# Kernel optimization log

Hardware: AMD Instinct MI355X
Metric: run time of the kernel (lower is better)

## Reference

```python
import jax, jax.numpy as jnp
import numpy as np

NEG = -1e9


def setup_inputs() -> dict:
    key = jax.random.key(0)
    kq, kk, kv, ke = jax.random.split(key, 4)
    B, H, S, D = 4, 16, 2048, 64
    q = jax.random.normal(kq, (B, H, S, D), dtype=jnp.float32)
    k = jax.random.normal(kk, (B, H, S, D), dtype=jnp.float32)
    v = jax.random.normal(kv, (B, H, S, D), dtype=jnp.float32)
    event_length = jax.random.randint(ke, (B,), 0, S, dtype=jnp.int32)
    return {"q": q, "k": k, "v": v, "event_length": event_length}


def reference(q, k, v, event_length):
    B, H, S, D = q.shape
    scale = jnp.sqrt(jnp.asarray(D, dtype=jnp.float32))
    # [b,h,s,q] scores
    scores = jnp.einsum('bhsd,bhqd->bhsq', q, k) / scale
    idx = jnp.arange(S)
    el = event_length[:, None]  # [B,1]
    valid = idx[None, :] < el   # [B,S]
    # mask[b,s,q] = valid[b,s] & valid[b,q]; broadcast over heads
    mask = (valid[:, None, :, None] & valid[:, None, None, :])  # [B,1,S,S]
    scores = jnp.where(mask, scores, NEG)
    attn = jax.nn.softmax(scores, axis=-1)
    # dropout p=0.0 (eval): identity
    out = jnp.einsum('bhsq,bhqd->bhsd', attn, v)
    return out
```

## Files before the change

### kernel.cpp

```cpp
#include <hip/hip_runtime.h>
#include <hip/hip_bf16.h>


#define SQ 2048
#define DH 64
#define NBH 64
#define TK 64
#define NTILE 32
#define TILE_B 8192
#define LDE 72
#define LVP 68

typedef __attribute__((ext_vector_type(4))) float f32x4;
typedef __attribute__((ext_vector_type(8))) short bf16x8;
typedef __attribute__((ext_vector_type(4))) unsigned int u32x4;
typedef __attribute__((ext_vector_type(2))) unsigned int u32x2;

__device__ __forceinline__ unsigned int pk2(float lo, float hi) {
    __hip_bfloat162 h = __float22bfloat162_rn(float2{lo, hi});
    union { __hip_bfloat162 h; unsigned int u; } c; c.h = h;
    return c.u;
}

__device__ __forceinline__ float bfu16_to_f(unsigned short s) {
    union { unsigned int u; float f; } c; c.u = ((unsigned int)s) << 16;
    return c.f;
}

__device__ __forceinline__ void async_cp16(const void* g, void* l) {
    __builtin_amdgcn_global_load_lds(
        (const __attribute__((address_space(1))) unsigned int*)g,
        (__attribute__((address_space(3))) unsigned int*)l, 16, 0, 0);
}


__global__ __launch_bounds__(256)
void convkv(const float* __restrict__ K, const float* __restrict__ V,
            const int* __restrict__ EL, float* __restrict__ MV,
            char* __restrict__ Kbt, char* __restrict__ Vbt) {
    const int bh = blockIdx.x >> 5;
    const int kt = blockIdx.x & 31;
    const int k0 = kt * TK;
    const int el = EL[bh >> 4];
    const int t = threadIdx.x;
    const int r  = t >> 2;
    const int dc = t & 3;

    __shared__ short LV[64][LVP];

    {
        const float* vp = V + ((size_t)bh * SQ + k0 + r) * DH + dc * 16;
        f32x4 a = *(const f32x4*)vp;
        f32x4 b = *(const f32x4*)(vp + 4);
        f32x4 c2 = *(const f32x4*)(vp + 8);
        f32x4 d2 = *(const f32x4*)(vp + 12);
        u32x4 w0, w1;
        w0[0] = pk2(a[0], a[1]);  w0[1] = pk2(a[2], a[3]);
        w0[2] = pk2(b[0], b[1]);  w0[3] = pk2(b[2], b[3]);
        w1[0] = pk2(c2[0], c2[1]); w1[1] = pk2(c2[2], c2[3]);
        w1[2] = pk2(d2[0], d2[1]); w1[3] = pk2(d2[2], d2[3]);
        *(u32x4*)&LV[r][dc * 16]     = w0;
        *(u32x4*)&LV[r][dc * 16 + 8] = w1;
    }

    if (k0 < el) {
        const float* kp = K + ((size_t)bh * SQ + k0 + r) * DH + dc * 16;
        f32x4 a = *(const f32x4*)kp;
        f32x4 b = *(const f32x4*)(kp + 4);
        f32x4 c2 = *(const f32x4*)(kp + 8);
        f32x4 d2 = *(const f32x4*)(kp + 12);
        u32x4 w0, w1;
        w0[0] = pk2(a[0], a[1]);  w0[1] = pk2(a[2], a[3]);
        w0[2] = pk2(b[0], b[1]);  w0[3] = pk2(b[2], b[3]);
        w1[0] = pk2(c2[0], c2[1]); w1[1] = pk2(c2[2], c2[3]);
        w1[2] = pk2(d2[0], d2[1]); w1[3] = pk2(d2[2], d2[3]);
        char* kb = Kbt + (size_t)(bh * NTILE + kt) * TILE_B + r * 128;
        *(u32x4*)(kb + (((dc * 2)     ^ (r & 7)) << 4)) = w0;
        *(u32x4*)(kb + (((dc * 2 + 1) ^ (r & 7)) << 4)) = w1;
    }

    __syncthreads();

    const int dd  = t >> 2;
    const int seg = t & 3;
    float msum = 0.f;
    unsigned int wv[8];
    #pragma unroll
    for (int i = 0; i < 8; ++i) {
        const int pos = seg * 16 + 2 * i;
        const int key = (pos & ~31) | ((pos & 4) << 2) | ((pos & 24) >> 1) | (pos & 3);
        const unsigned short s0 = (unsigned short)LV[key][dd];
        const unsigned short s1 = (unsigned short)LV[key + 1][dd];
        msum += bfu16_to_f(s0) + bfu16_to_f(s1);
        wv[i] = (unsigned int)s0 | ((unsigned int)s1 << 16);
    }
    msum += __shfl_xor(msum, 1);
    msum += __shfl_xor(msum, 2);
    if (seg == 0) atomicAdd(&MV[bh * DH + dd], msum * (1.0f / (float)SQ));

    if (k0 < el) {
        char* vb = Vbt + (size_t)(bh * NTILE + kt) * TILE_B + dd * 128;
        u32x4 o0 = {wv[0], wv[1], wv[2], wv[3]};
        u32x4 o1 = {wv[4], wv[5], wv[6], wv[7]};
        *(u32x4*)(vb + (((seg * 2)     ^ (dd & 7)) << 4)) = o0;
        *(u32x4*)(vb + (((seg * 2 + 1) ^ (dd & 7)) << 4)) = o1;
    }
}

__global__ __launch_bounds__(512, 4)
void flash6(const float* __restrict__ Q, const int* __restrict__ EL,
            const float* __restrict__ MV, float* __restrict__ O,
            const char* __restrict__ Kbt, const char* __restrict__ Vbt,
            int* __restrict__ ticket) {
    const int t = threadIdx.x;

    {
        const int bh0 = blockIdx.x & (NBH - 1);
        const int qb0 = (blockIdx.x >> 6) * 128;
        const int elb = EL[bh0 >> 4];
        if (qb0 >= elb) {
            float* Op = O + (size_t)bh0 * SQ * DH;
            const int c16 = t & 15, r0 = t >> 4;
            f32x4 mv = *(const f32x4*)(MV + bh0 * DH + c16 * 4);
            #pragma unroll
            for (int i = 0; i < 4; ++i)
                *(f32x4*)(Op + (size_t)(qb0 + r0 + i * 32) * DH + c16 * 4) = mv;
        }
    }

    const int el0 = EL[0], el1 = EL[1], el2 = EL[2], el3 = EL[3];
    const int v0 = (el0 + 127) >> 7, v1 = (el1 + 127) >> 7;
    const int v2 = (el2 + 127) >> 7, v3 = (el3 + 127) >> 7;
    const int n0 = 16 * v0, n1 = n0 + 16 * v1, n2 = n1 + 16 * v2;
    const int nvalid = n2 + 16 * v3;

    __shared__ short KT[2][TK * DH];
    __shared__ short VT[2][TK * DH];
    __shared__ int item_s;

    const int wq = t >> 6, lane = t & 63, qd = lane >> 4, c = lane & 15;
    const int cs = c & 7;

    for (;;) {
        if (t == 0) item_s = atomicAdd(ticket, 1);
        __syncthreads();
        const int it = item_s;
        if (it >= nvalid) break;

        int b, u, vb, el;
        if      (it < n0) { b = 0; u = it;      vb = v0; el = el0; }
        else if (it < n1) { b = 1; u = it - n0; vb = v1; el = el1; }
        else if (it < n2) { b = 2; u = it - n1; vb = v2; el = el2; }
        else              { b = 3; u = it - n2; vb = v3; el = el3; }
        const int head  = u / vb;
        const int qt    = u - head * vb;
        const int bh    = b * 16 + head;
        const int qbase = qt * 128;

        const float* Qp = Q + (size_t)bh * SQ * DH;
        float*       Op = O + (size_t)bh * SQ * DH;
        const char*  Kt = Kbt + (size_t)bh * NTILE * TILE_B;
        const char*  Vt = Vbt + (size_t)bh * NTILE * TILE_B;

        const float sc = 0.125f * 1.44269504f;
        const int qrow = qbase + wq * 16 + c;
        bf16x8 qf[2];
        #pragma unroll
        for (int kc = 0; kc < 2; ++kc) {
            const float* p = Qp + (size_t)qrow * DH + kc * 32 + qd * 8;
            f32x4 a  = *(const f32x4*)p;
            f32x4 bq = *(const f32x4*)(p + 4);
            u32x4 f;
            f[0] = pk2(a[0] * sc, a[1] * sc);
            f[1] = pk2(a[2] * sc, a[3] * sc);
            f[2] = pk2(bq[0] * sc, bq[1] * sc);
            f[3] = pk2(bq[2] * sc, bq[3] * sc);
            qf[kc] = *(bf16x8*)&f;
        }

        float l_ = 0.f;
        f32x4 oacc[4];
        #pragma unroll
        for (int dt = 0; dt < 4; ++dt) oacc[dt] = (f32x4){0.f, 0.f, 0.f, 0.f};

        const int nkt = (el + TK - 1) >> 6;

        {
            async_cp16(Kt + (size_t)t * 16, (char*)&KT[0][0] + wq * 1024);
            async_cp16(Vt + (size_t)t * 16, (char*)&VT[0][0] + wq * 1024);
        }
        asm volatile("s_waitcnt vmcnt(0)" ::: "memory");
        __syncthreads();

        int buf = 0;
        for (int kt = 0; kt < nkt; ++kt) {
            if (kt + 1 < nkt) {
                const char* gK = Kt + (size_t)(kt + 1) * TILE_B + t * 16;
                const char* gV = Vt + (size_t)(kt + 1) * TILE_B + t * 16;
                async_cp16(gK, (char*)&KT[buf ^ 1][0] + wq * 1024);
                async_cp16(gV, (char*)&VT[buf ^ 1][0] + wq * 1024);
            }
            const int k0 = kt * TK;

            const char* Kb = (const char*)&KT[buf][0];
            f32x4 st[4];
            #pragma unroll
            for (int mt = 0; mt < 4; ++mt) {
                const char* rp = Kb + (mt * 16 + c) * 128;
                bf16x8 a0 = *(const bf16x8*)(rp + (((qd)     ^ cs) << 4));
                bf16x8 a1 = *(const bf16x8*)(rp + (((qd + 4) ^ cs) << 4));
                f32x4 acc = (f32x4){0.f, 0.f, 0.f, 0.f};
                acc = __builtin_amdgcn_mfma_f32_16x16x32_bf16(a0, qf[0], acc, 0, 0, 0);
                acc = __builtin_amdgcn_mfma_f32_16x16x32_bf16(a1, qf[1], acc, 0, 0, 0);
                st[mt] = acc;
            }

            if (k0 + TK > el) {
                #pragma unroll
                for (int mt = 0; mt < 4; ++mt)
                    #pragma unroll
                    for (int r = 0; r < 4; ++r)
                        if (k0 + mt * 16 + qd * 4 + r >= el) st[mt][r] = -1e30f;
            }

            u32x4 pw[2];
            #pragma unroll
            for (int mt = 0; mt < 4; ++mt) {
                const float p0 = exp2f(st[mt][0]);
                const float p1 = exp2f(st[mt][1]);
                const float p2 = exp2f(st[mt][2]);
                const float p3 = exp2f(st[mt][3]);
                l_ += (p0 + p1) + (p2 + p3);
                pw[mt >> 1][(mt & 1) * 2]     = pk2(p0, p1);
                pw[mt >> 1][(mt & 1) * 2 + 1] = pk2(p2, p3);
            }

            const char* Vb = (const char*)&VT[buf][0];
            #pragma unroll
            for (int kc = 0; kc < 2; ++kc) {
                bf16x8 pb = *(bf16x8*)&pw[kc];
                #pragma unroll
                for (int dt = 0; dt < 4; ++dt) {
                    const char* vp = Vb + (dt * 16 + c) * 128 + (((kc * 4 + qd) ^ cs) << 4);
                    bf16x8 vf = *(const bf16x8*)vp;
                    oacc[dt] = __builtin_amdgcn_mfma_f32_16x16x32_bf16(vf, pb, oacc[dt], 0, 0, 0);
                }
            }

            asm volatile("s_waitcnt vmcnt(0)" ::: "memory");
            __syncthreads();
            buf ^= 1;
        }

        l_ += __shfl_xor(l_, 16);
        l_ += __shfl_xor(l_, 32);

        if (qrow < el) {
            const float inv = 1.0f / l_;
            #pragma unroll
            for (int dt = 0; dt < 4; ++dt) {
                f32x4 o = oacc[dt];
                o[0] *= inv; o[1] *= inv; o[2] *= inv; o[3] *= inv;
                *(f32x4*)(Op + (size_t)qrow * DH + dt * 16 + qd * 4) = o;
            }
        } else {
            #pragma unroll
            for (int dt = 0; dt < 4; ++dt)
                *(f32x4*)(Op + (size_t)qrow * DH + dt * 16 + qd * 4) =
                    *(const f32x4*)(MV + bh * DH + dt * 16 + qd * 4);
        }
    }
}


__global__ __launch_bounds__(256)
void meanv_k(const float* __restrict__ V, float* __restrict__ MV) {
    const int bh  = blockIdx.x >> 4;
    const int seg = blockIdx.x & 15;
    const float* vp = V + ((size_t)bh * SQ + (size_t)seg * 128) * DH;
    const int c = threadIdx.x & 15;
    const int r = threadIdx.x >> 4;
    const float* p = vp + (size_t)r * DH + c * 4;
    f32x4 s0 = *(const f32x4*)(p);
    f32x4 s1 = *(const f32x4*)(p + 16 * DH);
    f32x4 s2 = *(const f32x4*)(p + 32 * DH);
    f32x4 s3 = *(const f32x4*)(p + 48 * DH);
    s0 += *(const f32x4*)(p + 64 * DH);
    s1 += *(const f32x4*)(p + 80 * DH);
    s2 += *(const f32x4*)(p + 96 * DH);
    s3 += *(const f32x4*)(p + 112 * DH);
    f32x4 s = (s0 + s1) + (s2 + s3);
    __shared__ f32x4 red[16][16];
    red[r][c] = s;
    __syncthreads();
    if (threadIdx.x < 16) {
        f32x4 a = red[0][threadIdx.x];
        #pragma unroll
        for (int j = 1; j < 16; ++j) a += red[j][threadIdx.x];
        const float inv = 1.0f / (float)SQ;
        atomicAdd(&MV[bh * DH + threadIdx.x * 4 + 0], a[0] * inv);
        atomicAdd(&MV[bh * DH + threadIdx.x * 4 + 1], a[1] * inv);
        atomicAdd(&MV[bh * DH + threadIdx.x * 4 + 2], a[2] * inv);
        atomicAdd(&MV[bh * DH + threadIdx.x * 4 + 3], a[3] * inv);
    }
}

__global__ __launch_bounds__(256, 3)
void flash5(const float* __restrict__ Q, const float* __restrict__ K,
            const float* __restrict__ V, const int* __restrict__ EL,
            const float* __restrict__ MV, float* __restrict__ O,
            int* __restrict__ ticket) {
    const int t = threadIdx.x;
    {
        const int bh0    = blockIdx.x & (NBH - 1);
        const int qbase0 = (blockIdx.x >> 6) * 128;
        const int elb    = EL[bh0 >> 4];
        if (qbase0 >= elb) {
            float* Op = O + (size_t)bh0 * SQ * DH;
            const int c16 = t & 15, r0 = t >> 4;
            f32x4 mv = *(const f32x4*)(MV + bh0 * DH + c16 * 4);
            #pragma unroll
            for (int i = 0; i < 8; ++i)
                *(f32x4*)(Op + (size_t)(qbase0 + r0 + i * 16) * DH + c16 * 4) = mv;
        }
    }

    const int el0 = EL[0], el1 = EL[1], el2 = EL[2], el3 = EL[3];
    const int v0 = (el0 + 127) >> 7, v1 = (el1 + 127) >> 7;
    const int v2 = (el2 + 127) >> 7, v3 = (el3 + 127) >> 7;
    const int n0 = 16 * v0, n1 = n0 + 16 * v1, n2 = n1 + 16 * v2;
    const int nvalid = n2 + 16 * v3;

    __shared__ short Kb[TK][LDE];
    __shared__ short Vt[DH][LDE];
    __shared__ short Pl[4][32][LDE];
    __shared__ int item_s;

    const int wq = t >> 6, lane = t & 63, qd = lane >> 4, c = lane & 15;
    const int ksrow = t >> 2;
    const int ksdc  = t & 3;
    const int vpair = t & 31;
    const int vdg   = t >> 5;

    for (;;) {
        if (t == 0) item_s = atomicAdd(ticket, 1);
        __syncthreads();
        const int it = item_s;
        if (it >= nvalid) break;

        int b, u, vb, el;
        if      (it < n0) { b = 0; u = it;      vb = v0; el = el0; }
        else if (it < n1) { b = 1; u = it - n0; vb = v1; el = el1; }
        else if (it < n2) { b = 2; u = it - n1; vb = v2; el = el2; }
        else              { b = 3; u = it - n2; vb = v3; el = el3; }
        const int head  = u / vb;
        const int qt    = u - head * vb;
        const int bh    = b * 16 + head;
        const int qbase = qt * 128;

        const size_t base = (size_t)bh * SQ * DH;
        const float* Qp = Q + base;
        const float* Kp = K + base;
        const float* Vp = V + base;
        float* Op = O + base;

        const float sc = 0.125f * 1.44269504f;
        bf16x8 qf[2][2];
        #pragma unroll
        for (int nt = 0; nt < 2; ++nt) {
            const int row = qbase + wq * 32 + nt * 16 + c;
            #pragma unroll
            for (int kc = 0; kc < 2; ++kc) {
                const float* p = Qp + (size_t)row * DH + kc * 32 + qd * 8;
                f32x4 a  = *(const f32x4*)p;
                f32x4 bb = *(const f32x4*)(p + 4);
                u32x4 f;
                f[0] = pk2(a[0] * sc, a[1] * sc);
                f[1] = pk2(a[2] * sc, a[3] * sc);
                f[2] = pk2(bb[0] * sc, bb[1] * sc);
                f[3] = pk2(bb[2] * sc, bb[3] * sc);
                qf[nt][kc] = *(bf16x8*)&f;
            }
        }

        float l_[2] = {0.f, 0.f};
        f32x4 oacc[4][2];
        #pragma unroll
        for (int dt = 0; dt < 4; ++dt)
            #pragma unroll
            for (int nt = 0; nt < 2; ++nt)
                oacc[dt][nt] = (f32x4){0.f, 0.f, 0.f, 0.f};

        const int nkt = (el + TK - 1) / TK;

        f32x4 kg0, kg1, kg2, kg3, vg0, vg1, vg2, vg3;
        {
            const float* kp = Kp + (size_t)ksrow * DH + ksdc * 16;
            kg0 = *(const f32x4*)kp;
            kg1 = *(const f32x4*)(kp + 4);
            kg2 = *(const f32x4*)(kp + 8);
            kg3 = *(const f32x4*)(kp + 12);
            const float* vp0 = Vp + (size_t)(2 * vpair) * DH + vdg * 8;
            vg0 = *(const f32x4*)vp0;
            vg1 = *(const f32x4*)(vp0 + 4);
            vg2 = *(const f32x4*)(vp0 + DH);
            vg3 = *(const f32x4*)(vp0 + DH + 4);
        }

        for (int kt = 0; kt < nkt; ++kt) {
            const int k0 = kt * TK;

            __syncthreads();
            {
                u32x4 w0, w1;
                w0[0] = pk2(kg0[0], kg0[1]); w0[1] = pk2(kg0[2], kg0[3]);
                w0[2] = pk2(kg1[0], kg1[1]); w0[3] = pk2(kg1[2], kg1[3]);
                w1[0] = pk2(kg2[0], kg2[1]); w1[1] = pk2(kg2[2], kg2[3]);
                w1[2] = pk2(kg3[0], kg3[1]); w1[3] = pk2(kg3[2], kg3[3]);
                *(u32x4*)&Kb[ksrow][ksdc * 16]     = w0;
                *(u32x4*)&Kb[ksrow][ksdc * 16 + 8] = w1;
            }
            {
                #pragma unroll
                for (int i = 0; i < 4; ++i) {
                    *(unsigned int*)&Vt[vdg * 8 + i][2 * vpair]     = pk2(vg0[i], vg2[i]);
                    *(unsigned int*)&Vt[vdg * 8 + 4 + i][2 * vpair] = pk2(vg1[i], vg3[i]);
                }
            }
            __syncthreads();

            if (kt + 1 < nkt) {
                const int kn = k0 + TK;
                const float* kp = Kp + (size_t)(kn + ksrow) * DH + ksdc * 16;
                kg0 = *(const f32x4*)kp;
                kg1 = *(const f32x4*)(kp + 4);
                kg2 = *(const f32x4*)(kp + 8);
                kg3 = *(const f32x4*)(kp + 12);
                const float* vp0 = Vp + (size_t)(kn + 2 * vpair) * DH + vdg * 8;
                vg0 = *(const f32x4*)vp0;
                vg1 = *(const f32x4*)(vp0 + 4);
                vg2 = *(const f32x4*)(vp0 + DH);
                vg3 = *(const f32x4*)(vp0 + DH + 4);
            }

            f32x4 st[4][2];
            #pragma unroll
            for (int mt = 0; mt < 4; ++mt) {
                bf16x8 a0 = *(const bf16x8*)&Kb[mt * 16 + c][qd * 8];
                bf16x8 a1 = *(const bf16x8*)&Kb[mt * 16 + c][32 + qd * 8];
                #pragma unroll
                for (int nt = 0; nt < 2; ++nt) {
                    f32x4 acc = (f32x4){0.f, 0.f, 0.f, 0.f};
                    acc = __builtin_amdgcn_mfma_f32_16x16x32_bf16(a0, qf[nt][0], acc, 0, 0, 0);
                    acc = __builtin_amdgcn_mfma_f32_16x16x32_bf16(a1, qf[nt][1], acc, 0, 0, 0);
                    st[mt][nt] = acc;
                }
            }

            if (k0 + TK > el) {
                #pragma unroll
                for (int mt = 0; mt < 4; ++mt)
                    #pragma unroll
                    for (int r = 0; r < 4; ++r)
                        if (k0 + mt * 16 + qd * 4 + r >= el) {
                            st[mt][0][r] = -1e30f;
                            st[mt][1][r] = -1e30f;
                        }
            }

            #pragma unroll
            for (int nt = 0; nt < 2; ++nt) {
                #pragma unroll
                for (int mt = 0; mt < 4; ++mt) {
                    const float p0 = exp2f(st[mt][nt][0]);
                    const float p1 = exp2f(st[mt][nt][1]);
                    const float p2 = exp2f(st[mt][nt][2]);
                    const float p3 = exp2f(st[mt][nt][3]);
                    l_[nt] += (p0 + p1) + (p2 + p3);
                    u32x2 pw;
                    pw[0] = pk2(p0, p1);
                    pw[1] = pk2(p2, p3);
                    *(u32x2*)&Pl[wq][nt * 16 + c][mt * 16 + qd * 4] = pw;
                }
            }

            #pragma unroll
            for (int kc = 0; kc < 2; ++kc) {
                bf16x8 pb0 = *(const bf16x8*)&Pl[wq][c][kc * 32 + qd * 8];
                bf16x8 pb1 = *(const bf16x8*)&Pl[wq][16 + c][kc * 32 + qd * 8];
                #pragma unroll
                for (int dt = 0; dt < 4; ++dt) {
                    bf16x8 vf = *(const bf16x8*)&Vt[dt * 16 + c][kc * 32 + qd * 8];
                    oacc[dt][0] = __builtin_amdgcn_mfma_f32_16x16x32_bf16(vf, pb0, oacc[dt][0], 0, 0, 0);
                    oacc[dt][1] = __builtin_amdgcn_mfma_f32_16x16x32_bf16(vf, pb1, oacc[dt][1], 0, 0, 0);
                }
            }
        }

        #pragma unroll
        for (int nt = 0; nt < 2; ++nt) {
            l_[nt] += __shfl_xor(l_[nt], 16);
            l_[nt] += __shfl_xor(l_[nt], 32);
        }

        #pragma unroll
        for (int nt = 0; nt < 2; ++nt) {
            const int row = qbase + wq * 32 + nt * 16 + c;
            if (row < el) {
                const float inv = 1.0f / l_[nt];
                #pragma unroll
                for (int dt = 0; dt < 4; ++dt) {
                    f32x4 o = oacc[dt][nt];
                    o[0] *= inv; o[1] *= inv; o[2] *= inv; o[3] *= inv;
                    *(f32x4*)(Op + (size_t)row * DH + dt * 16 + qd * 4) = o;
                }
            } else {
                #pragma unroll
                for (int dt = 0; dt < 4; ++dt) {
                    f32x4 mv = *(const f32x4*)(MV + bh * DH + dt * 16 + qd * 4);
                    *(f32x4*)(Op + (size_t)row * DH + dt * 16 + qd * 4) = mv;
                }
            }
        }
    }
}


extern "C" void kernel_launch(void* const* d_in, const int* in_sizes, int n_in,
                              void* d_out, int out_size, void* d_ws, size_t ws_size,
                              hipStream_t stream) {
    const float* q  = (const float*)d_in[0];
    const float* k  = (const float*)d_in[1];
    const float* v  = (const float*)d_in[2];
    const int*   el = (const int*)d_in[3];
    float* out = (float*)d_out;

    const size_t kbt_bytes = (size_t)NBH * NTILE * TILE_B;
    const size_t needed    = 65536 + 2 * kbt_bytes;

    if (ws_size >= needed) {
        float* mv  = (float*)d_ws;
        int*   tk  = (int*)((char*)d_ws + 16384);
        char*  kbt = (char*)d_ws + 65536;
        char*  vbt = kbt + kbt_bytes;

        hipMemsetAsync(d_ws, 0, 65536, stream);
        convkv<<<dim3(NBH * NTILE), dim3(256), 0, stream>>>(k, v, el, mv, kbt, vbt);
        flash6<<<dim3(NBH * (SQ / 128)), dim3(512), 0, stream>>>(q, el, mv, out, kbt, vbt, tk);
    } else {
        float* mv = (float*)d_ws;
        int*   tk = (int*)((char*)d_ws + NBH * DH * sizeof(float));

        hipMemsetAsync(d_ws, 0, NBH * DH * sizeof(float) + 64, stream);
        meanv_k<<<dim3(NBH * 16), dim3(256), 0, stream>>>(v, mv);
        flash5<<<dim3(NBH * (SQ / 128)), dim3(256), 0, stream>>>(q, k, v, el, mv, out, tk);
    }
}
```

Measured before the change: 194.2 us.

## Process two query sub-tiles per wave with 256-thread blocks to reuse K/V fragments

Each wave now handles 32 query rows (two 16-row sub-tiles) instead of 16, and the block shrinks from 512 to 256 threads. Every K and V fragment read from LDS feeds two MFMAs, halving LDS reads per unit of compute, and each thread issues two async copies per tile to keep the 64-key K/V tile fully loaded. The softmax exp also switches to the raw hardware exp2 builtin. Costs are higher register pressure (twice the accumulators, scores and Q fragments) and fewer waves per block to hide latency.

```diff
diff --git a/kernel.cpp b/kernel.cpp
--- a/kernel.cpp
+++ b/kernel.cpp
@@ -107,8 +107,8 @@
     }
 }
 
-__global__ __launch_bounds__(512, 4)
-void flash6(const float* __restrict__ Q, const int* __restrict__ EL,
+__global__ __launch_bounds__(256, 4)
+void flash7(const float* __restrict__ Q, const int* __restrict__ EL,
             const float* __restrict__ MV, float* __restrict__ O,
             const char* __restrict__ Kbt, const char* __restrict__ Vbt,
             int* __restrict__ ticket) {
@@ -123,8 +123,8 @@
             const int c16 = t & 15, r0 = t >> 4;
             f32x4 mv = *(const f32x4*)(MV + bh0 * DH + c16 * 4);
             #pragma unroll
-            for (int i = 0; i < 4; ++i)
-                *(f32x4*)(Op + (size_t)(qb0 + r0 + i * 32) * DH + c16 * 4) = mv;
+            for (int i = 0; i < 8; ++i)
+                *(f32x4*)(Op + (size_t)(qb0 + r0 + i * 16) * DH + c16 * 4) = mv;
         }
     }
 
@@ -163,31 +163,39 @@
         const char*  Vt = Vbt + (size_t)bh * NTILE * TILE_B;
 
         const float sc = 0.125f * 1.44269504f;
-        const int qrow = qbase + wq * 16 + c;
-        bf16x8 qf[2];
-        #pragma unroll
-        for (int kc = 0; kc < 2; ++kc) {
-            const float* p = Qp + (size_t)qrow * DH + kc * 32 + qd * 8;
-            f32x4 a  = *(const f32x4*)p;
-            f32x4 bq = *(const f32x4*)(p + 4);
-            u32x4 f;
-            f[0] = pk2(a[0] * sc, a[1] * sc);
-            f[1] = pk2(a[2] * sc, a[3] * sc);
-            f[2] = pk2(bq[0] * sc, bq[1] * sc);
-            f[3] = pk2(bq[2] * sc, bq[3] * sc);
-            qf[kc] = *(bf16x8*)&f;
-        }
-
-        float l_ = 0.f;
-        f32x4 oacc[4];
-        #pragma unroll
-        for (int dt = 0; dt < 4; ++dt) oacc[dt] = (f32x4){0.f, 0.f, 0.f, 0.f};
+        bf16x8 qf[2][2];
+        #pragma unroll
+        for (int nt = 0; nt < 2; ++nt) {
+            const int row = qbase + wq * 32 + nt * 16 + c;
+            #pragma unroll
+            for (int kc = 0; kc < 2; ++kc) {
+                const float* p = Qp + (size_t)row * DH + kc * 32 + qd * 8;
+                f32x4 a  = *(const f32x4*)p;
+                f32x4 bq = *(const f32x4*)(p + 4);
+                u32x4 f;
+                f[0] = pk2(a[0] * sc, a[1] * sc);
+                f[1] = pk2(a[2] * sc, a[3] * sc);
+                f[2] = pk2(bq[0] * sc, bq[1] * sc);
+                f[3] = pk2(bq[2] * sc, bq[3] * sc);
+                qf[nt][kc] = *(bf16x8*)&f;
+            }
+        }
+
+        float l_[2] = {0.f, 0.f};
+        f32x4 oacc[4][2];
+        #pragma unroll
+        for (int dt = 0; dt < 4; ++dt) {
+            oacc[dt][0] = (f32x4){0.f, 0.f, 0.f, 0.f};
+            oacc[dt][1] = (f32x4){0.f, 0.f, 0.f, 0.f};
+        }
 
         const int nkt = (el + TK - 1) >> 6;
 
         {
-            async_cp16(Kt + (size_t)t * 16, (char*)&KT[0][0] + wq * 1024);
-            async_cp16(Vt + (size_t)t * 16, (char*)&VT[0][0] + wq * 1024);
+            async_cp16(Kt + (size_t)t * 16,        (char*)&KT[0][0] + wq * 1024);
+            async_cp16(Kt + 4096 + (size_t)t * 16, (char*)&KT[0][0] + 4096 + wq * 1024);
+            async_cp16(Vt + (size_t)t * 16,        (char*)&VT[0][0] + wq * 1024);
+            async_cp16(Vt + 4096 + (size_t)t * 16, (char*)&VT[0][0] + 4096 + wq * 1024);
         }
         asm volatile("s_waitcnt vmcnt(0)" ::: "memory");
         __syncthreads();
@@ -197,22 +205,29 @@
             if (kt + 1 < nkt) {
                 const char* gK = Kt + (size_t)(kt + 1) * TILE_B + t * 16;
                 const char* gV = Vt + (size_t)(kt + 1) * TILE_B + t * 16;
-                async_cp16(gK, (char*)&KT[buf ^ 1][0] + wq * 1024);
-                async_cp16(gV, (char*)&VT[buf ^ 1][0] + wq * 1024);
+                char* lK = (char*)&KT[buf ^ 1][0] + wq * 1024;
+                char* lV = (char*)&VT[buf ^ 1][0] + wq * 1024;
+                async_cp16(gK,        lK);
+                async_cp16(gK + 4096, lK + 4096);
+                async_cp16(gV,        lV);
+                async_cp16(gV + 4096, lV + 4096);
             }
             const int k0 = kt * TK;
 
             const char* Kb = (const char*)&KT[buf][0];
-            f32x4 st[4];
+            f32x4 st[4][2];
             #pragma unroll
             for (int mt = 0; mt < 4; ++mt) {
                 const char* rp = Kb + (mt * 16 + c) * 128;
                 bf16x8 a0 = *(const bf16x8*)(rp + (((qd)     ^ cs) << 4));
                 bf16x8 a1 = *(const bf16x8*)(rp + (((qd + 4) ^ cs) << 4));
-                f32x4 acc = (f32x4){0.f, 0.f, 0.f, 0.f};
-                acc = __builtin_amdgcn_mfma_f32_16x16x32_bf16(a0, qf[0], acc, 0, 0, 0);
-                acc = __builtin_amdgcn_mfma_f32_16x16x32_bf16(a1, qf[1], acc, 0, 0, 0);
-                st[mt] = acc;
+                #pragma unroll
+                for (int nt = 0; nt < 2; ++nt) {
+                    f32x4 acc = (f32x4){0.f, 0.f, 0.f, 0.f};
+                    acc = __builtin_amdgcn_mfma_f32_16x16x32_bf16(a0, qf[nt][0], acc, 0, 0, 0);
+                    acc = __builtin_amdgcn_mfma_f32_16x16x32_bf16(a1, qf[nt][1], acc, 0, 0, 0);
+                    st[mt][nt] = acc;
+                }
             }
 
             if (k0 + TK > el) {
@@ -220,30 +235,38 @@
                 for (int mt = 0; mt < 4; ++mt)
                     #pragma unroll
                     for (int r = 0; r < 4; ++r)
-                        if (k0 + mt * 16 + qd * 4 + r >= el) st[mt][r] = -1e30f;
-            }
-
-            u32x4 pw[2];
-            #pragma unroll
-            for (int mt = 0; mt < 4; ++mt) {
-                const float p0 = exp2f(st[mt][0]);
-                const float p1 = exp2f(st[mt][1]);
-                const float p2 = exp2f(st[mt][2]);
-                const float p3 = exp2f(st[mt][3]);
-                l_ += (p0 + p1) + (p2 + p3);
-                pw[mt >> 1][(mt & 1) * 2]     = pk2(p0, p1);
-                pw[mt >> 1][(mt & 1) * 2 + 1] = pk2(p2, p3);
+                        if (k0 + mt * 16 + qd * 4 + r >= el) {
+                            st[mt][0][r] = -1e30f;
+                            st[mt][1][r] = -1e30f;
+                        }
+            }
+
+            u32x4 pw[2][2];
+            #pragma unroll
+            for (int nt = 0; nt < 2; ++nt) {
+                #pragma unroll
+                for (int mt = 0; mt < 4; ++mt) {
+                    const float p0 = __builtin_amdgcn_exp2f(st[mt][nt][0]);
+                    const float p1 = __builtin_amdgcn_exp2f(st[mt][nt][1]);
+                    const float p2 = __builtin_amdgcn_exp2f(st[mt][nt][2]);
+                    const float p3 = __builtin_amdgcn_exp2f(st[mt][nt][3]);
+                    l_[nt] += (p0 + p1) + (p2 + p3);
+                    pw[nt][mt >> 1][(mt & 1) * 2]     = pk2(p0, p1);
+                    pw[nt][mt >> 1][(mt & 1) * 2 + 1] = pk2(p2, p3);
+                }
             }
 
             const char* Vb = (const char*)&VT[buf][0];
             #pragma unroll
             for (int kc = 0; kc < 2; ++kc) {
-                bf16x8 pb = *(bf16x8*)&pw[kc];
+                bf16x8 pb0 = *(bf16x8*)&pw[0][kc];
+                bf16x8 pb1 = *(bf16x8*)&pw[1][kc];
                 #pragma unroll
                 for (int dt = 0; dt < 4; ++dt) {
                     const char* vp = Vb + (dt * 16 + c) * 128 + (((kc * 4 + qd) ^ cs) << 4);
                     bf16x8 vf = *(const bf16x8*)vp;
-                    oacc[dt] = __builtin_amdgcn_mfma_f32_16x16x32_bf16(vf, pb, oacc[dt], 0, 0, 0);
+                    oacc[dt][0] = __builtin_amdgcn_mfma_f32_16x16x32_bf16(vf, pb0, oacc[dt][0], 0, 0, 0);
+                    oacc[dt][1] = __builtin_amdgcn_mfma_f32_16x16x32_bf16(vf, pb1, oacc[dt][1], 0, 0, 0);
                 }
             }
 
@@ -252,22 +275,29 @@
             buf ^= 1;
         }
 
-        l_ += __shfl_xor(l_, 16);
-        l_ += __shfl_xor(l_, 32);
-
-        if (qrow < el) {
-            const float inv = 1.0f / l_;
-            #pragma unroll
-            for (int dt = 0; dt < 4; ++dt) {
-                f32x4 o = oacc[dt];
-                o[0] *= inv; o[1] *= inv; o[2] *= inv; o[3] *= inv;
-                *(f32x4*)(Op + (size_t)qrow * DH + dt * 16 + qd * 4) = o;
-            }
-        } else {
-            #pragma unroll
-            for (int dt = 0; dt < 4; ++dt)
-                *(f32x4*)(Op + (size_t)qrow * DH + dt * 16 + qd * 4) =
-                    *(const f32x4*)(MV + bh * DH + dt * 16 + qd * 4);
+        #pragma unroll
+        for (int nt = 0; nt < 2; ++nt) {
+            l_[nt] += __shfl_xor(l_[nt], 16);
+            l_[nt] += __shfl_xor(l_[nt], 32);
+        }
+
+        #pragma unroll
+        for (int nt = 0; nt < 2; ++nt) {
+            const int qrow = qbase + wq * 32 + nt * 16 + c;
+            if (qrow < el) {
+                const float inv = 1.0f / l_[nt];
+                #pragma unroll
+                for (int dt = 0; dt < 4; ++dt) {
+                    f32x4 o = oacc[dt][nt];
+                    o[0] *= inv; o[1] *= inv; o[2] *= inv; o[3] *= inv;
+                    *(f32x4*)(Op + (size_t)qrow * DH + dt * 16 + qd * 4) = o;
+                }
+            } else {
+                #pragma unroll
+                for (int dt = 0; dt < 4; ++dt)
+                    *(f32x4*)(Op + (size_t)qrow * DH + dt * 16 + qd * 4) =
+                        *(const f32x4*)(MV + bh * DH + dt * 16 + qd * 4);
+            }
         }
     }
 }
@@ -546,7 +576,7 @@
 
         hipMemsetAsync(d_ws, 0, 65536, stream);
         convkv<<<dim3(NBH * NTILE), dim3(256), 0, stream>>>(k, v, el, mv, kbt, vbt);
-        flash6<<<dim3(NBH * (SQ / 128)), dim3(512), 0, stream>>>(q, el, mv, out, kbt, vbt, tk);
+        flash7<<<dim3(NBH * (SQ / 128)), dim3(256), 0, stream>>>(q, el, mv, out, kbt, vbt, tk);
     } else {
         float* mv = (float*)d_ws;
         int*   tk = (int*)((char*)d_ws + NBH * DH * sizeof(float));
```

After: 197.2 us. About the same (+1.6%).

## Triple-buffer K/V tiles with fragment-ordered layout and prefetch depth two

Applied to the files above, without the earlier changes.

The K/V conversion kernel now writes tiles in MFMA fragment order, so each lane reads its operands with contiguous 16-byte loads at fixed offsets and no XOR swizzle. The flash kernel moves from double to triple-buffered LDS with two tiles in flight and partial vmcnt waits. It also issues the first loads before the Q fragment setup, raises the occupancy hint, uses the raw exp2 builtin and brackets the MFMA blocks with setprio. The aim is to hide global-to-LDS latency and cut LDS address math, at the cost of 48KB of LDS per block, which may limit occupancy, and an extra barrier per iteration.

```diff
diff --git a/kernel.cpp b/kernel.cpp
--- a/kernel.cpp
+++ b/kernel.cpp
@@ -15,6 +15,8 @@
 typedef __attribute__((ext_vector_type(8))) short bf16x8;
 typedef __attribute__((ext_vector_type(4))) unsigned int u32x4;
 typedef __attribute__((ext_vector_type(2))) unsigned int u32x2;
+
+#define VMCNT(n) asm volatile("s_waitcnt vmcnt(" #n ")" ::: "memory")
 
 __device__ __forceinline__ unsigned int pk2(float lo, float hi) {
     __hip_bfloat162 h = __float22bfloat162_rn(float2{lo, hi});
@@ -74,9 +76,12 @@
         w0[2] = pk2(b[0], b[1]);  w0[3] = pk2(b[2], b[3]);
         w1[0] = pk2(c2[0], c2[1]); w1[1] = pk2(c2[2], c2[3]);
         w1[2] = pk2(d2[0], d2[1]); w1[3] = pk2(d2[2], d2[3]);
-        char* kb = Kbt + (size_t)(bh * NTILE + kt) * TILE_B + r * 128;
-        *(u32x4*)(kb + (((dc * 2)     ^ (r & 7)) << 4)) = w0;
-        *(u32x4*)(kb + (((dc * 2 + 1) ^ (r & 7)) << 4)) = w1;
+        char* kb = Kbt + (size_t)(bh * NTILE + kt) * TILE_B;
+        const int fi  = (r >> 4) * 2 + (dc >> 1);
+        const int qd0 = (dc & 1) * 2;
+        char* d0 = kb + fi * 1024 + qd0 * 256 + (r & 15) * 16;
+        *(u32x4*)d0         = w0;
+        *(u32x4*)(d0 + 256) = w1;
     }
 
     __syncthreads();
@@ -99,16 +104,19 @@
     if (seg == 0) atomicAdd(&MV[bh * DH + dd], msum * (1.0f / (float)SQ));
 
     if (k0 < el) {
-        char* vb = Vbt + (size_t)(bh * NTILE + kt) * TILE_B + dd * 128;
+        char* vbb = Vbt + (size_t)(bh * NTILE + kt) * TILE_B;
+        const int fi  = (seg >> 1) * 4 + (dd >> 4);
+        const int qd0 = (seg & 1) * 2;
+        char* d0 = vbb + fi * 1024 + qd0 * 256 + (dd & 15) * 16;
         u32x4 o0 = {wv[0], wv[1], wv[2], wv[3]};
         u32x4 o1 = {wv[4], wv[5], wv[6], wv[7]};
-        *(u32x4*)(vb + (((seg * 2)     ^ (dd & 7)) << 4)) = o0;
-        *(u32x4*)(vb + (((seg * 2 + 1) ^ (dd & 7)) << 4)) = o1;
-    }
-}
-
-__global__ __launch_bounds__(512, 4)
-void flash6(const float* __restrict__ Q, const int* __restrict__ EL,
+        *(u32x4*)d0         = o0;
+        *(u32x4*)(d0 + 256) = o1;
+    }
+}
+
+__global__ __launch_bounds__(512, 6)
+void flash9(const float* __restrict__ Q, const int* __restrict__ EL,
             const float* __restrict__ MV, float* __restrict__ O,
             const char* __restrict__ Kbt, const char* __restrict__ Vbt,
             int* __restrict__ ticket) {
@@ -134,12 +142,12 @@
     const int n0 = 16 * v0, n1 = n0 + 16 * v1, n2 = n1 + 16 * v2;
     const int nvalid = n2 + 16 * v3;
 
-    __shared__ short KT[2][TK * DH];
-    __shared__ short VT[2][TK * DH];
+    __shared__ char KB[3 * TILE_B];
+    __shared__ char VB[3 * TILE_B];
     __shared__ int item_s;
 
     const int wq = t >> 6, lane = t & 63, qd = lane >> 4, c = lane & 15;
-    const int cs = c & 7;
+    const float sc = 0.125f * 1.44269504f;
 
     for (;;) {
         if (t == 0) item_s = atomicAdd(ticket, 1);
@@ -159,10 +167,20 @@
 
         const float* Qp = Q + (size_t)bh * SQ * DH;
         float*       Op = O + (size_t)bh * SQ * DH;
-        const char*  Kt = Kbt + (size_t)bh * NTILE * TILE_B;
-        const char*  Vt = Vbt + (size_t)bh * NTILE * TILE_B;
-
-        const float sc = 0.125f * 1.44269504f;
+        const char*  Kt = Kbt + (size_t)bh * NTILE * TILE_B + t * 16;
+        const char*  Vt = Vbt + (size_t)bh * NTILE * TILE_B + t * 16;
+        char* const  kdst = KB + wq * 1024;
+        char* const  vdst = VB + wq * 1024;
+
+        const int nkt = (el + TK - 1) >> 6;
+
+        async_cp16(Kt, kdst);
+        async_cp16(Vt, vdst);
+        if (nkt > 1) {
+            async_cp16(Kt + TILE_B, kdst + TILE_B);
+            async_cp16(Vt + TILE_B, vdst + TILE_B);
+        }
+
         const int qrow = qbase + wq * 16 + c;
         bf16x8 qf[2];
         #pragma unroll
@@ -183,38 +201,40 @@
         #pragma unroll
         for (int dt = 0; dt < 4; ++dt) oacc[dt] = (f32x4){0.f, 0.f, 0.f, 0.f};
 
-        const int nkt = (el + TK - 1) >> 6;
-
-        {
-            async_cp16(Kt + (size_t)t * 16, (char*)&KT[0][0] + wq * 1024);
-            async_cp16(Vt + (size_t)t * 16, (char*)&VT[0][0] + wq * 1024);
-        }
-        asm volatile("s_waitcnt vmcnt(0)" ::: "memory");
-        __syncthreads();
-
-        int buf = 0;
         for (int kt = 0; kt < nkt; ++kt) {
-            if (kt + 1 < nkt) {
-                const char* gK = Kt + (size_t)(kt + 1) * TILE_B + t * 16;
-                const char* gV = Vt + (size_t)(kt + 1) * TILE_B + t * 16;
-                async_cp16(gK, (char*)&KT[buf ^ 1][0] + wq * 1024);
-                async_cp16(gV, (char*)&VT[buf ^ 1][0] + wq * 1024);
-            }
+            const int s = kt % 3;
+
+            __syncthreads();
+            if (kt + 2 < nkt) {
+                const int s2 = (kt + 2) % 3;
+                async_cp16(Kt + (size_t)(kt + 2) * TILE_B, kdst + s2 * TILE_B);
+                async_cp16(Vt + (size_t)(kt + 2) * TILE_B, vdst + s2 * TILE_B);
+            }
+            if      (kt + 2 < nkt) VMCNT(4);
+            else if (kt + 1 < nkt) VMCNT(2);
+            else                   VMCNT(0);
+            __syncthreads();
+
+            const char* Kb = KB + s * TILE_B + lane * 16;
+            const char* Vb = VB + s * TILE_B + lane * 16;
+
+            bf16x8 ka[8];
+            #pragma unroll
+            for (int i = 0; i < 8; ++i)
+                ka[i] = *(const bf16x8*)(Kb + i * 1024);
+
+            f32x4 st[4];
+            __builtin_amdgcn_s_setprio(1);
+            #pragma unroll
+            for (int mt = 0; mt < 4; ++mt) {
+                f32x4 acc = (f32x4){0.f, 0.f, 0.f, 0.f};
+                acc = __builtin_amdgcn_mfma_f32_16x16x32_bf16(ka[mt*2],   qf[0], acc, 0, 0, 0);
+                acc = __builtin_amdgcn_mfma_f32_16x16x32_bf16(ka[mt*2+1], qf[1], acc, 0, 0, 0);
+                st[mt] = acc;
+            }
+            __builtin_amdgcn_s_setprio(0);
+
             const int k0 = kt * TK;
-
-            const char* Kb = (const char*)&KT[buf][0];
-            f32x4 st[4];
-            #pragma unroll
-            for (int mt = 0; mt < 4; ++mt) {
-                const char* rp = Kb + (mt * 16 + c) * 128;
-                bf16x8 a0 = *(const bf16x8*)(rp + (((qd)     ^ cs) << 4));
-                bf16x8 a1 = *(const bf16x8*)(rp + (((qd + 4) ^ cs) << 4));
-                f32x4 acc = (f32x4){0.f, 0.f, 0.f, 0.f};
-                acc = __builtin_amdgcn_mfma_f32_16x16x32_bf16(a0, qf[0], acc, 0, 0, 0);
-                acc = __builtin_amdgcn_mfma_f32_16x16x32_bf16(a1, qf[1], acc, 0, 0, 0);
-                st[mt] = acc;
-            }
-
             if (k0 + TK > el) {
                 #pragma unroll
                 for (int mt = 0; mt < 4; ++mt)
@@ -226,30 +246,29 @@
             u32x4 pw[2];
             #pragma unroll
             for (int mt = 0; mt < 4; ++mt) {
-                const float p0 = exp2f(st[mt][0]);
-                const float p1 = exp2f(st[mt][1]);
-                const float p2 = exp2f(st[mt][2]);
-                const float p3 = exp2f(st[mt][3]);
+                const float p0 = __builtin_amdgcn_exp2f(st[mt][0]);
+                const float p1 = __builtin_amdgcn_exp2f(st[mt][1]);
+                const float p2 = __builtin_amdgcn_exp2f(st[mt][2]);
+                const float p3 = __builtin_amdgcn_exp2f(st[mt][3]);
                 l_ += (p0 + p1) + (p2 + p3);
                 pw[mt >> 1][(mt & 1) * 2]     = pk2(p0, p1);
                 pw[mt >> 1][(mt & 1) * 2 + 1] = pk2(p2, p3);
             }
 
-            const char* Vb = (const char*)&VT[buf][0];
+            bf16x8 va[8];
+            #pragma unroll
+            for (int i = 0; i < 8; ++i)
+                va[i] = *(const bf16x8*)(Vb + i * 1024);
+
+            __builtin_amdgcn_s_setprio(1);
             #pragma unroll
             for (int kc = 0; kc < 2; ++kc) {
                 bf16x8 pb = *(bf16x8*)&pw[kc];
                 #pragma unroll
-                for (int dt = 0; dt < 4; ++dt) {
-                    const char* vp = Vb + (dt * 16 + c) * 128 + (((kc * 4 + qd) ^ cs) << 4);
-                    bf16x8 vf = *(const bf16x8*)vp;
-                    oacc[dt] = __builtin_amdgcn_mfma_f32_16x16x32_bf16(vf, pb, oacc[dt], 0, 0, 0);
-                }
-            }
-
-            asm volatile("s_waitcnt vmcnt(0)" ::: "memory");
-            __syncthreads();
-            buf ^= 1;
+                for (int dt = 0; dt < 4; ++dt)
+                    oacc[dt] = __builtin_amdgcn_mfma_f32_16x16x32_bf16(va[kc*4+dt], pb, oacc[dt], 0, 0, 0);
+            }
+            __builtin_amdgcn_s_setprio(0);
         }
 
         l_ += __shfl_xor(l_, 16);
@@ -546,7 +565,7 @@
 
         hipMemsetAsync(d_ws, 0, 65536, stream);
         convkv<<<dim3(NBH * NTILE), dim3(256), 0, stream>>>(k, v, el, mv, kbt, vbt);
-        flash6<<<dim3(NBH * (SQ / 128)), dim3(512), 0, stream>>>(q, el, mv, out, kbt, vbt, tk);
+        flash9<<<dim3(NBH * (SQ / 128)), dim3(512), 0, stream>>>(q, el, mv, out, kbt, vbt, tk);
     } else {
         float* mv = (float*)d_ws;
         int*   tk = (int*)((char*)d_ws + NBH * DH * sizeof(float));
```

Measured after the change: 198.3 us. 2.1% more time.
